# Kernel optimization log

Hardware: AMD Instinct MI355X
Metric: run time of the kernel (lower is better)

The kernel has to match this reference:

```python
import jax, jax.numpy as jnp
import numpy as np

HEADS = 16

def setup_inputs() -> dict:
    key = jax.random.key(0)
    k1, k2, k3 = jax.random.split(key, 3)
    T, B, E = 2048, 4, 1024
    query = jax.random.normal(k1, (T, B, E), dtype=jnp.float32)
    in_proj_weight = jax.random.normal(k2, (3 * E, E), dtype=jnp.float32) * (E ** -0.5)
    out_proj_weight = jax.random.normal(k3, (E, E), dtype=jnp.float32) * (E ** -0.5)
    return {"query": query, "in_proj_weight": in_proj_weight, "out_proj_weight": out_proj_weight}

def reference(query, in_proj_weight, out_proj_weight):
    # query: [T, B, E] (time-first, as in apex SelfMultiheadAttn)
    T, B, E = query.shape
    H = HEADS
    D = E // H
    scale = D ** -0.5
    # fused in-projection: x @ W_in^T -> [T, B, 3E]
    qkv = jnp.einsum('tbe,fe->tbf', query, in_proj_weight)
    q, k, v = jnp.split(qkv, 3, axis=-1)
    # [T, B, E] -> [B, H, T, D]
    def to_bhtd(x):
        return x.reshape(T, B, H, D).transpose(1, 2, 0, 3)
    q = to_bhtd(q) * scale
    k = to_bhtd(k)
    v = to_bhtd(v)
    scores = jnp.einsum('bhqd,bhkd->bhqk', q, k)  # [B, H, T, T]
    # causal (mask_future_timesteps=True) time mask
    causal = jnp.tril(jnp.ones((T, T), dtype=bool))
    scores = jnp.where(causal, scores, jnp.finfo(scores.dtype).min)
    attn = jax.nn.softmax(scores, axis=-1)
    # dropout_prob = 0.0 -> identity
    ctx = jnp.einsum('bhqk,bhkd->bhqd', attn, v)  # [B, H, T, D]
    ctx = ctx.transpose(2, 0, 1, 3).reshape(T, B, E)
    out = jnp.einsum('tbe,fe->tbf', ctx, out_proj_weight)
    return out
```

## Files before the change

### kernel.cpp

```cpp
#include <hip/hip_runtime.h>


typedef float  f32x4  __attribute__((ext_vector_type(4)));
typedef short  s16x8  __attribute__((ext_vector_type(8)));
typedef __bf16 bf16x8 __attribute__((ext_vector_type(8)));

#define T_DIM 2048
#define B_DIM 4
#define E_DIM 1024
#define PLANE (T_DIM * 64)

#define VMC(N) asm volatile("s_waitcnt vmcnt(" #N ")" ::: "memory")
#define LGKM0() asm volatile("s_waitcnt lgkmcnt(0)" ::: "memory")
#define BAR() __builtin_amdgcn_s_barrier()

__device__ inline unsigned short f2bf(float f) {
  return (unsigned short)((__builtin_bit_cast(unsigned int, f) + 0x8000u) >> 16);
}

__device__ inline f32x4 mfma16(s16x8 a, s16x8 b, f32x4 c) {
  return __builtin_amdgcn_mfma_f32_16x16x32_bf16(
      __builtin_bit_cast(bf16x8, a), __builtin_bit_cast(bf16x8, b), c, 0, 0, 0);
}

__device__ inline void gl2lds16(const unsigned short* g, unsigned short* l) {
  __builtin_amdgcn_global_load_lds(
      (__attribute__((address_space(1))) unsigned int*)g,
      (__attribute__((address_space(3))) unsigned int*)l, 16, 0, 0);
}

__device__ inline unsigned packbf(float a, float b) {
  return __builtin_amdgcn_perm(__builtin_bit_cast(unsigned, b),
                               __builtin_bit_cast(unsigned, a), 0x07060302u);
}

__global__ __launch_bounds__(256)
void cvt_all(const float* __restrict__ q, const float* __restrict__ wi,
             const float* __restrict__ wo, unsigned short* __restrict__ xb,
             unsigned short* __restrict__ wib, unsigned short* __restrict__ wob,
             float qs, int do_wout) {
  int blk = blockIdx.x;
  const float* src;
  unsigned short* dst;
  int i;
  float sc = 1.0f;
  if (blk < 8192) {
    src = q; dst = xb; i = blk * 256 + threadIdx.x;
  } else if (blk < 11264) {
    src = wi; dst = wib; i = (blk - 8192) * 256 + threadIdx.x;
    if (i < (E_DIM * E_DIM / 4)) sc = qs;
  } else {
    if (!do_wout) return;
    src = wo; dst = wob; i = (blk - 11264) * 256 + threadIdx.x;
  }
  float4 v = ((const float4*)src)[i];
  ushort4 o;
  o.x = f2bf(v.x * sc); o.y = f2bf(v.y * sc);
  o.z = f2bf(v.z * sc); o.w = f2bf(v.w * sc);
  ((ushort4*)dst)[i] = o;
}

__global__ __launch_bounds__(256)
void cvt_bf16(const float* __restrict__ in, unsigned short* __restrict__ out,
              int n4) {
  int i = blockIdx.x * 256 + threadIdx.x;
  if (i >= n4) return;
  float4 v = ((const float4*)in)[i];
  ushort4 o;
  o.x = f2bf(v.x); o.y = f2bf(v.y); o.z = f2bf(v.z); o.w = f2bf(v.w);
  ((ushort4*)out)[i] = o;
}

__global__ __launch_bounds__(256)
void gemm_qkv(const unsigned short* __restrict__ A,
              const unsigned short* __restrict__ Bw,
              unsigned short* __restrict__ Cq, int K) {
  __shared__ __attribute__((aligned(16))) unsigned short As[2][8192];
  __shared__ __attribute__((aligned(16))) unsigned short Bs[2][8192];

  const int tid = threadIdx.x, lane = tid & 63, w = tid >> 6;
  const int row16 = lane & 15, quad = lane >> 4;
  const int m0 = blockIdx.y * 128, n0 = blockIdx.x * 128;
  const int wm = (w & 1) * 64, wn = (w >> 1) * 64;
  const int srow = lane >> 3;
  const int jsw = (lane & 7) ^ srow;
  const int sw7 = row16 & 7;

  f32x4 acc[4][4];
  for (int i = 0; i < 4; ++i)
    for (int j = 0; j < 4; ++j) acc[i][j] = (f32x4){0.f, 0.f, 0.f, 0.f};

  auto stage = [&](int kt, int buf) {
#pragma unroll
    for (int i = 0; i < 4; ++i) {
      int ia = i * 4 + w;
      int r = ia * 8 + srow;
      gl2lds16(A  + (size_t)(m0 + r) * K + kt * 64 + jsw * 8,
               &As[buf][ia * 512]);
      gl2lds16(Bw + (size_t)(n0 + r) * K + kt * 64 + jsw * 8,
               &Bs[buf][ia * 512]);
    }
  };

  const int NT = K / 64;
  stage(0, 0);
  stage(1, 1);

  for (int kt = 0; kt < NT; ++kt) {
    const int buf = kt & 1;
    if (kt < NT - 1) VMC(8);
    else             VMC(0);
    BAR();

    for (int kk = 0; kk < 2; ++kk) {
      s16x8 af[4], bfr[4];
      for (int mi = 0; mi < 4; ++mi)
        af[mi] = *(const s16x8*)&As[buf][(wm + mi * 16 + row16) * 64 +
                                         (((kk * 4 + quad) ^ sw7) * 8)];
      for (int ni = 0; ni < 4; ++ni)
        bfr[ni] = *(const s16x8*)&Bs[buf][(wn + ni * 16 + row16) * 64 +
                                          (((kk * 4 + quad) ^ sw7) * 8)];
      for (int mi = 0; mi < 4; ++mi)
        for (int ni = 0; ni < 4; ++ni)
          acc[mi][ni] = mfma16(af[mi], bfr[ni], acc[mi][ni]);
    }

    BAR();
    if (kt + 2 < NT) stage(kt + 2, buf);
  }

  if (n0 >= 2048) {
    const int hw = ((n0 - 2048) >> 6) + (w >> 1);
    const int tg0 = (m0 >> 2) + (w & 1) * 16;
    unsigned short* tb = &As[0][0] + w * 1536;
    for (int bb = 0; bb < 4; ++bb) {
#pragma unroll
      for (int mi = 0; mi < 4; ++mi)
#pragma unroll
        for (int ni = 0; ni < 4; ++ni)
          tb[(ni * 16 + row16) * 24 + mi * 4 + quad] = f2bf(acc[mi][ni][bb]);
      LGKM0();
      unsigned short* vp = Cq + (size_t)(128 + bb * 16 + hw) * PLANE;
#pragma unroll
      for (int it = 0; it < 2; ++it) {
        int dd = it * 32 + (lane >> 1);
        int tl = (lane & 1) * 8;
        s16x8 v = *(const s16x8*)&tb[dd * 24 + tl];
        *(s16x8*)(vp + (size_t)dd * T_DIM + tg0 + tl) = v;
      }
      LGKM0();
    }
  } else {
    for (int mi = 0; mi < 4; ++mi)
      for (int ni = 0; ni < 4; ++ni)
        for (int r = 0; r < 4; ++r) {
          int m = m0 + wm + mi * 16 + quad * 4 + r;
          int n = n0 + wn + ni * 16 + row16;
          int t = m >> 2, bb = m & 3;
          int which = n >> 10, hh = (n >> 6) & 15, dd = n & 63;
          Cq[(size_t)(which * 64 + bb * 16 + hh) * PLANE + (size_t)t * 64 + dd] =
              f2bf(acc[mi][ni][r]);
        }
  }
}

__global__ __launch_bounds__(256)
void gemm128(const unsigned short* __restrict__ A,
             const unsigned short* __restrict__ Bw,
             float* __restrict__ Cf, int N, int K) {
  __shared__ __attribute__((aligned(16))) unsigned short As[128 * 64];
  __shared__ __attribute__((aligned(16))) unsigned short Bs[128 * 64];

  const int tid = threadIdx.x, lane = tid & 63, w = tid >> 6;
  const int row16 = lane & 15, quad = lane >> 4;
  const int m0 = blockIdx.y * 128, n0 = blockIdx.x * 128;
  const int wm = (w & 1) * 64, wn = (w >> 1) * 64;
  const int srow = lane >> 3;
  const int jsw = (lane & 7) ^ srow;
  const int sw7 = row16 & 7;

  f32x4 acc[4][4];
  for (int i = 0; i < 4; ++i)
    for (int j = 0; j < 4; ++j) acc[i][j] = (f32x4){0.f, 0.f, 0.f, 0.f};

  for (int k0 = 0; k0 < K; k0 += 64) {
    for (int i = 0; i < 4; ++i) {
      int ia = i * 4 + w;
      int r = ia * 8 + srow;
      gl2lds16(A  + (size_t)(m0 + r) * K + k0 + jsw * 8, &As[ia * 512]);
      gl2lds16(Bw + (size_t)(n0 + r) * K + k0 + jsw * 8, &Bs[ia * 512]);
    }
    __syncthreads();
    for (int kk = 0; kk < 2; ++kk) {
      s16x8 af[4], bfr[4];
      for (int mi = 0; mi < 4; ++mi)
        af[mi] = *(const s16x8*)&As[(wm + mi * 16 + row16) * 64 +
                                    (((kk * 4 + quad) ^ sw7) * 8)];
      for (int ni = 0; ni < 4; ++ni)
        bfr[ni] = *(const s16x8*)&Bs[(wn + ni * 16 + row16) * 64 +
                                     (((kk * 4 + quad) ^ sw7) * 8)];
      for (int mi = 0; mi < 4; ++mi)
        for (int ni = 0; ni < 4; ++ni)
          acc[mi][ni] = mfma16(af[mi], bfr[ni], acc[mi][ni]);
    }
    __syncthreads();
  }

  for (int mi = 0; mi < 4; ++mi)
    for (int ni = 0; ni < 4; ++ni)
      for (int r = 0; r < 4; ++r) {
        int m = m0 + wm + mi * 16 + quad * 4 + r;
        int n = n0 + wn + ni * 16 + row16;
        Cf[(size_t)m * N + n] = acc[mi][ni][r];
      }
}

__global__ __launch_bounds__(512, 4)
void attn_fwd(const unsigned short* __restrict__ qkv,
              unsigned short* __restrict__ ctx) {
  __shared__ __attribute__((aligned(16))) unsigned short Ks[2][4096];
  __shared__ __attribute__((aligned(16))) unsigned short Vs[2][4096];
  __shared__ __attribute__((aligned(16))) unsigned short Ps[8][1024];

  const int tid = threadIdx.x, lane = tid & 63, w = tid >> 6;
  const int row16 = lane & 15, quad = lane >> 4;
  const int bh = blockIdx.x;
  const int p  = blockIdx.y;
  const int b = bh >> 4, h = bh & 15;

  const unsigned short* Qg = qkv + (size_t)bh * PLANE;
  const unsigned short* Kg = qkv + (size_t)(64 + bh) * PLANE;
  const unsigned short* Vt = qkv + (size_t)(128 + bh) * PLANE;

  const int r8 = lane >> 3;
  const int jsw = (lane & 7) ^ r8;
  const int sw7 = row16 & 7;

  auto stage = [&](int c, int buf) {
    int r = w * 8 + r8;
    gl2lds16(Kg + (size_t)(c * 64 + r) * 64 + jsw * 8, &Ks[buf][w * 512]);
    gl2lds16(Vt + (size_t)r * T_DIM + c * 64 + jsw * 8, &Vs[buf][w * 512]);
  };

  for (int half = 0; half < 2; ++half) {
    const int qt = half ? p : (15 - p);
    const int q0w = qt * 128 + w * 16;
    const int cmax = 2 * qt + 1;
    const int dc = 2 * qt + (w >> 2);

    s16x8 qb[2];
    for (int s = 0; s < 2; ++s)
      qb[s] = *(const s16x8*)(Qg + (size_t)(q0w + row16) * 64 + s * 32 +
                              quad * 8);

    f32x4 O[4];
    for (int md = 0; md < 4; ++md) O[md] = (f32x4){0.f, 0.f, 0.f, 0.f};
    float lp = 0.f;

    stage(0, 0);
    stage(1, 1);

    for (int c = 0; c <= cmax; ++c) {
      const int buf = c & 1;
      if (c < cmax) VMC(2);
      else          VMC(0);
      BAR();

      if (c <= dc) {
        f32x4 S[4];
        for (int nt = 0; nt < 4; ++nt) S[nt] = (f32x4){0.f, 0.f, 0.f, 0.f};
        __builtin_amdgcn_s_setprio(1);
        for (int nt = 0; nt < 4; ++nt)
          for (int s = 0; s < 2; ++s) {
            s16x8 ka = *(const s16x8*)&Ks[buf][(nt * 16 + row16) * 64 +
                                              (((s * 4 + quad) ^ sw7) * 8)];
            S[nt] = mfma16(ka, qb[s], S[nt]);
          }
        __builtin_amdgcn_s_setprio(0);

        const int qg = q0w + row16;
        auto softmax_store = [&](bool diagm) {
          for (int nt = 0; nt < 4; ++nt) {
            float pv[4];
            for (int r = 0; r < 4; ++r) {
              pv[r] = __builtin_amdgcn_exp2f(S[nt][r]);
              if (diagm && (c * 64 + nt * 16 + quad * 4 + r) > qg) pv[r] = 0.f;
              lp += pv[r];
            }
            int pos = (nt * 2 + (quad >> 1)) ^ sw7;
            *(uint2*)&Ps[w][row16 * 64 + pos * 8 + (quad & 1) * 4] =
                make_uint2(packbf(pv[0], pv[1]), packbf(pv[2], pv[3]));
          }
        };
        if (c == dc) softmax_store(true); else softmax_store(false);
        LGKM0();

        __builtin_amdgcn_s_setprio(1);
        for (int sk = 0; sk < 2; ++sk) {
          s16x8 pb = *(const s16x8*)&Ps[w][row16 * 64 +
                                          (((sk * 4 + quad) ^ sw7) * 8)];
          for (int md = 0; md < 4; ++md) {
            s16x8 va = *(const s16x8*)&Vs[buf][(md * 16 + row16) * 64 +
                                              (((sk * 4 + quad) ^ sw7) * 8)];
            O[md] = mfma16(va, pb, O[md]);
          }
        }
        __builtin_amdgcn_s_setprio(0);
      }

      BAR();
      if (c + 2 <= cmax) stage(c + 2, buf);
    }

    {
      float s = lp;
      s += __shfl_xor(s, 16);
      s += __shfl_xor(s, 32);
      float inv = 1.f / s;
      const int t = q0w + row16;
      for (int md = 0; md < 4; ++md) {
        unsigned lo = packbf(O[md][0] * inv, O[md][1] * inv);
        unsigned hi = packbf(O[md][2] * inv, O[md][3] * inv);
        *(uint2*)&ctx[((size_t)t * B_DIM + b) * E_DIM + h * 64 + md * 16 +
                      quad * 4] = make_uint2(lo, hi);
      }
    }
  }
}

extern "C" void kernel_launch(void* const* d_in, const int* in_sizes, int n_in,
                              void* d_out, int out_size, void* d_ws,
                              size_t ws_size, hipStream_t stream) {
  const float* query = (const float*)d_in[0];
  const float* win   = (const float*)d_in[1];
  const float* wout  = (const float*)d_in[2];
  float* out = (float*)d_out;

  const size_t qkv_el = (size_t)3 * 64 * PLANE;
  const size_t ctx_el = (size_t)T_DIM * B_DIM * E_DIM;

  unsigned short* qkvb = (unsigned short*)d_ws;
  unsigned short* ctxb = qkvb + qkv_el;
  unsigned short* xb   = ctxb;
  unsigned short* winb = (unsigned short*)d_out;

  const bool big_ws = ws_size >= (qkv_el + ctx_el + (size_t)E_DIM * E_DIM) * 2;
  unsigned short* woutb = big_ws ? (ctxb + ctx_el) : qkvb;

  const float QSCALE = 0.18033688011112042f;

  cvt_all<<<big_ws ? 12288 : 11264, 256, 0, stream>>>(
      query, win, wout, xb, winb, woutb, QSCALE, big_ws ? 1 : 0);
  gemm_qkv<<<dim3(3072 / 128, 8192 / 128), 256, 0, stream>>>(xb, winb, qkvb,
                                                             1024);
  attn_fwd<<<dim3(64, 8), 512, 0, stream>>>(qkvb, ctxb);
  if (!big_ws)
    cvt_bf16<<<1024, 256, 0, stream>>>(wout, woutb, (1024 * 1024) / 4);
  gemm128<<<dim3(8, 64), 256, 0, stream>>>(ctxb, woutb, out, 1024, 1024);
}
```

Measured before the change: 227.3 us.

## Use 8-wave QKV GEMM with MFMA priority and pipeline the out-projection GEMM

The QKV projection GEMM now runs 512 threads per block, each wave owning a 32x64 subtile, with s_setprio raised around the MFMA bursts. The V-transpose epilogue is reworked for the smaller per-wave tile. The output projection GEMM switches from a single-buffered, syncthreads-based loop to the double-buffered async-load pipeline. The aim is higher occupancy and better overlap of loads with MFMA, at the cost of more LDS per block and a lower MFMA-to-LDS-read ratio per wave.

```diff
diff --git a/kernel.cpp b/kernel.cpp
--- a/kernel.cpp
+++ b/kernel.cpp
@@ -71,10 +71,103 @@
   ((ushort4*)out)[i] = o;
 }
 
-__global__ __launch_bounds__(256)
+__global__ __launch_bounds__(512, 4)
 void gemm_qkv(const unsigned short* __restrict__ A,
               const unsigned short* __restrict__ Bw,
               unsigned short* __restrict__ Cq, int K) {
+  __shared__ __attribute__((aligned(16))) unsigned short As[2][8192];
+  __shared__ __attribute__((aligned(16))) unsigned short Bs[2][8192];
+
+  const int tid = threadIdx.x, lane = tid & 63, w = tid >> 6;
+  const int row16 = lane & 15, quad = lane >> 4;
+  const int m0 = blockIdx.y * 128, n0 = blockIdx.x * 128;
+  const int wm = (w & 3) * 32, wn = (w >> 2) * 64;
+  const int srow = lane >> 3;
+  const int jsw = (lane & 7) ^ srow;
+  const int sw7 = row16 & 7;
+
+  f32x4 acc[2][4];
+  for (int i = 0; i < 2; ++i)
+    for (int j = 0; j < 4; ++j) acc[i][j] = (f32x4){0.f, 0.f, 0.f, 0.f};
+
+  auto stage = [&](int kt, int buf) {
+#pragma unroll
+    for (int i = 0; i < 2; ++i) {
+      int ia = w * 2 + i;
+      int r = ia * 8 + srow;
+      gl2lds16(A  + (size_t)(m0 + r) * K + kt * 64 + jsw * 8,
+               &As[buf][ia * 512]);
+      gl2lds16(Bw + (size_t)(n0 + r) * K + kt * 64 + jsw * 8,
+               &Bs[buf][ia * 512]);
+    }
+  };
+
+  const int NT = K / 64;
+  stage(0, 0);
+  stage(1, 1);
+
+  for (int kt = 0; kt < NT; ++kt) {
+    const int buf = kt & 1;
+    if (kt < NT - 1) VMC(4);
+    else             VMC(0);
+    BAR();
+
+    for (int kk = 0; kk < 2; ++kk) {
+      s16x8 af[2], bfr[4];
+      for (int mi = 0; mi < 2; ++mi)
+        af[mi] = *(const s16x8*)&As[buf][(wm + mi * 16 + row16) * 64 +
+                                         (((kk * 4 + quad) ^ sw7) * 8)];
+      for (int ni = 0; ni < 4; ++ni)
+        bfr[ni] = *(const s16x8*)&Bs[buf][(wn + ni * 16 + row16) * 64 +
+                                          (((kk * 4 + quad) ^ sw7) * 8)];
+      __builtin_amdgcn_s_setprio(1);
+      for (int mi = 0; mi < 2; ++mi)
+        for (int ni = 0; ni < 4; ++ni)
+          acc[mi][ni] = mfma16(af[mi], bfr[ni], acc[mi][ni]);
+      __builtin_amdgcn_s_setprio(0);
+    }
+
+    BAR();
+    if (kt + 2 < NT) stage(kt + 2, buf);
+  }
+
+  if (n0 >= 2048) {
+    const int hw = ((n0 - 2048) >> 6) + (w >> 2);
+    const int tg0 = (m0 >> 2) + (w & 3) * 8;
+    unsigned short* tb = &As[0][0] + w * 768;
+    for (int bb = 0; bb < 4; ++bb) {
+#pragma unroll
+      for (int mi = 0; mi < 2; ++mi)
+#pragma unroll
+        for (int ni = 0; ni < 4; ++ni)
+          tb[(ni * 16 + row16) * 12 + mi * 4 + quad] = f2bf(acc[mi][ni][bb]);
+      LGKM0();
+      unsigned short* vp = Cq + (size_t)(128 + bb * 16 + hw) * PLANE;
+      {
+        int dd = lane;
+        s16x8 v = *(const s16x8*)&tb[dd * 12];
+        *(s16x8*)(vp + (size_t)dd * T_DIM + tg0) = v;
+      }
+      LGKM0();
+    }
+  } else {
+    for (int mi = 0; mi < 2; ++mi)
+      for (int ni = 0; ni < 4; ++ni)
+        for (int r = 0; r < 4; ++r) {
+          int m = m0 + wm + mi * 16 + quad * 4 + r;
+          int n = n0 + wn + ni * 16 + row16;
+          int t = m >> 2, bb = m & 3;
+          int which = n >> 10, hh = (n >> 6) & 15, dd = n & 63;
+          Cq[(size_t)(which * 64 + bb * 16 + hh) * PLANE + (size_t)t * 64 + dd] =
+              f2bf(acc[mi][ni][r]);
+        }
+  }
+}
+
+__global__ __launch_bounds__(256)
+void gemm128(const unsigned short* __restrict__ A,
+             const unsigned short* __restrict__ Bw,
+             float* __restrict__ Cf, int N, int K) {
   __shared__ __attribute__((aligned(16))) unsigned short As[2][8192];
   __shared__ __attribute__((aligned(16))) unsigned short Bs[2][8192];
 
@@ -127,83 +220,6 @@
 
     BAR();
     if (kt + 2 < NT) stage(kt + 2, buf);
-  }
-
-  if (n0 >= 2048) {
-    const int hw = ((n0 - 2048) >> 6) + (w >> 1);
-    const int tg0 = (m0 >> 2) + (w & 1) * 16;
-    unsigned short* tb = &As[0][0] + w * 1536;
-    for (int bb = 0; bb < 4; ++bb) {
-#pragma unroll
-      for (int mi = 0; mi < 4; ++mi)
-#pragma unroll
-        for (int ni = 0; ni < 4; ++ni)
-          tb[(ni * 16 + row16) * 24 + mi * 4 + quad] = f2bf(acc[mi][ni][bb]);
-      LGKM0();
-      unsigned short* vp = Cq + (size_t)(128 + bb * 16 + hw) * PLANE;
-#pragma unroll
-      for (int it = 0; it < 2; ++it) {
-        int dd = it * 32 + (lane >> 1);
-        int tl = (lane & 1) * 8;
-        s16x8 v = *(const s16x8*)&tb[dd * 24 + tl];
-        *(s16x8*)(vp + (size_t)dd * T_DIM + tg0 + tl) = v;
-      }
-      LGKM0();
-    }
-  } else {
-    for (int mi = 0; mi < 4; ++mi)
-      for (int ni = 0; ni < 4; ++ni)
-        for (int r = 0; r < 4; ++r) {
-          int m = m0 + wm + mi * 16 + quad * 4 + r;
-          int n = n0 + wn + ni * 16 + row16;
-          int t = m >> 2, bb = m & 3;
-          int which = n >> 10, hh = (n >> 6) & 15, dd = n & 63;
-          Cq[(size_t)(which * 64 + bb * 16 + hh) * PLANE + (size_t)t * 64 + dd] =
-              f2bf(acc[mi][ni][r]);
-        }
-  }
-}
-
-__global__ __launch_bounds__(256)
-void gemm128(const unsigned short* __restrict__ A,
-             const unsigned short* __restrict__ Bw,
-             float* __restrict__ Cf, int N, int K) {
-  __shared__ __attribute__((aligned(16))) unsigned short As[128 * 64];
-  __shared__ __attribute__((aligned(16))) unsigned short Bs[128 * 64];
-
-  const int tid = threadIdx.x, lane = tid & 63, w = tid >> 6;
-  const int row16 = lane & 15, quad = lane >> 4;
-  const int m0 = blockIdx.y * 128, n0 = blockIdx.x * 128;
-  const int wm = (w & 1) * 64, wn = (w >> 1) * 64;
-  const int srow = lane >> 3;
-  const int jsw = (lane & 7) ^ srow;
-  const int sw7 = row16 & 7;
-
-  f32x4 acc[4][4];
-  for (int i = 0; i < 4; ++i)
-    for (int j = 0; j < 4; ++j) acc[i][j] = (f32x4){0.f, 0.f, 0.f, 0.f};
-
-  for (int k0 = 0; k0 < K; k0 += 64) {
-    for (int i = 0; i < 4; ++i) {
-      int ia = i * 4 + w;
-      int r = ia * 8 + srow;
-      gl2lds16(A  + (size_t)(m0 + r) * K + k0 + jsw * 8, &As[ia * 512]);
-      gl2lds16(Bw + (size_t)(n0 + r) * K + k0 + jsw * 8, &Bs[ia * 512]);
-    }
-    __syncthreads();
-    for (int kk = 0; kk < 2; ++kk) {
-      s16x8 af[4], bfr[4];
-      for (int mi = 0; mi < 4; ++mi)
-        af[mi] = *(const s16x8*)&As[(wm + mi * 16 + row16) * 64 +
-                                    (((kk * 4 + quad) ^ sw7) * 8)];
-      for (int ni = 0; ni < 4; ++ni)
-        bfr[ni] = *(const s16x8*)&Bs[(wn + ni * 16 + row16) * 64 +
-                                     (((kk * 4 + quad) ^ sw7) * 8)];
-      for (int mi = 0; mi < 4; ++mi)
-        for (int ni = 0; ni < 4; ++ni)
-          acc[mi][ni] = mfma16(af[mi], bfr[ni], acc[mi][ni]);
-    }
-    __syncthreads();
   }
 
   for (int mi = 0; mi < 4; ++mi)
@@ -351,7 +367,7 @@
 
   cvt_all<<<big_ws ? 12288 : 11264, 256, 0, stream>>>(
       query, win, wout, xb, winb, woutb, QSCALE, big_ws ? 1 : 0);
-  gemm_qkv<<<dim3(3072 / 128, 8192 / 128), 256, 0, stream>>>(xb, winb, qkvb,
+  gemm_qkv<<<dim3(3072 / 128, 8192 / 128), 512, 0, stream>>>(xb, winb, qkvb,
                                                              1024);
   attn_fwd<<<dim3(64, 8), 512, 0, stream>>>(qkvb, ctxb);
   if (!big_ws)
```

New measurement: 227.2 us. About the same (-0.0%).

## Shrink QKV GEMM K-tile to 32 for occupancy; double-buffer out-proj GEMM

Applied to the files above, without the earlier changes.

The QKV projection GEMM now stages 32-wide K tiles, which halves its LDS footprint. It gets a new XOR swizzle, launch bounds requesting 4 blocks per CU, and s_setprio around the MFMA burst. The output-projection GEMM (gemm128) takes over the previous double-buffered 64-wide pipeline with vmcnt waits in place of its single-buffered __syncthreads loop. The aim is more resident waves for the QKV GEMM and overlap of loads with compute in the out-projection. The trade-off is twice as many barriers per K in the QKV GEMM and more LDS in gemm128.

```diff
diff --git a/kernel.cpp b/kernel.cpp
--- a/kernel.cpp
+++ b/kernel.cpp
@@ -71,10 +71,102 @@
   ((ushort4*)out)[i] = o;
 }
 
-__global__ __launch_bounds__(256)
+__global__ __launch_bounds__(256, 4)
 void gemm_qkv(const unsigned short* __restrict__ A,
               const unsigned short* __restrict__ Bw,
               unsigned short* __restrict__ Cq, int K) {
+  __shared__ __attribute__((aligned(16))) unsigned short As[2][4096];
+  __shared__ __attribute__((aligned(16))) unsigned short Bs[2][4096];
+
+  const int tid = threadIdx.x, lane = tid & 63, w = tid >> 6;
+  const int row16 = lane & 15, quad = lane >> 4;
+  const int m0 = blockIdx.y * 128, n0 = blockIdx.x * 128;
+  const int wm = (w & 1) * 64, wn = (w >> 1) * 64;
+  const int jsw = (lane & 3) ^ ((lane >> 3) & 3);
+  const int csw = (row16 >> 1) & 3;
+
+  f32x4 acc[4][4];
+  for (int i = 0; i < 4; ++i)
+    for (int j = 0; j < 4; ++j) acc[i][j] = (f32x4){0.f, 0.f, 0.f, 0.f};
+
+  auto stage = [&](int kt, int buf) {
+#pragma unroll
+    for (int i = 0; i < 2; ++i) {
+      int ia = i * 4 + w;
+      int r = ia * 16 + (lane >> 2);
+      gl2lds16(A  + (size_t)(m0 + r) * K + kt * 32 + jsw * 8,
+               &As[buf][ia * 512]);
+      gl2lds16(Bw + (size_t)(n0 + r) * K + kt * 32 + jsw * 8,
+               &Bs[buf][ia * 512]);
+    }
+  };
+
+  const int NT = K / 32;
+  stage(0, 0);
+  stage(1, 1);
+
+  for (int kt = 0; kt < NT; ++kt) {
+    const int buf = kt & 1;
+    if (kt < NT - 1) VMC(4);
+    else             VMC(0);
+    BAR();
+
+    s16x8 af[4], bfr[4];
+    for (int mi = 0; mi < 4; ++mi)
+      af[mi] = *(const s16x8*)&As[buf][(wm + mi * 16 + row16) * 32 +
+                                       ((quad ^ csw) * 8)];
+    for (int ni = 0; ni < 4; ++ni)
+      bfr[ni] = *(const s16x8*)&Bs[buf][(wn + ni * 16 + row16) * 32 +
+                                        ((quad ^ csw) * 8)];
+    __builtin_amdgcn_s_setprio(1);
+    for (int mi = 0; mi < 4; ++mi)
+      for (int ni = 0; ni < 4; ++ni)
+        acc[mi][ni] = mfma16(af[mi], bfr[ni], acc[mi][ni]);
+    __builtin_amdgcn_s_setprio(0);
+
+    BAR();
+    if (kt + 2 < NT) stage(kt + 2, buf);
+  }
+
+  if (n0 >= 2048) {
+    const int hw = ((n0 - 2048) >> 6) + (w >> 1);
+    const int tg0 = (m0 >> 2) + (w & 1) * 16;
+    unsigned short* tb = &As[0][0] + w * 1536;
+    for (int bb = 0; bb < 4; ++bb) {
+#pragma unroll
+      for (int mi = 0; mi < 4; ++mi)
+#pragma unroll
+        for (int ni = 0; ni < 4; ++ni)
+          tb[(ni * 16 + row16) * 24 + mi * 4 + quad] = f2bf(acc[mi][ni][bb]);
+      LGKM0();
+      unsigned short* vp = Cq + (size_t)(128 + bb * 16 + hw) * PLANE;
+#pragma unroll
+      for (int it = 0; it < 2; ++it) {
+        int dd = it * 32 + (lane >> 1);
+        int tl = (lane & 1) * 8;
+        s16x8 v = *(const s16x8*)&tb[dd * 24 + tl];
+        *(s16x8*)(vp + (size_t)dd * T_DIM + tg0 + tl) = v;
+      }
+      LGKM0();
+    }
+  } else {
+    for (int mi = 0; mi < 4; ++mi)
+      for (int ni = 0; ni < 4; ++ni)
+        for (int r = 0; r < 4; ++r) {
+          int m = m0 + wm + mi * 16 + quad * 4 + r;
+          int n = n0 + wn + ni * 16 + row16;
+          int t = m >> 2, bb = m & 3;
+          int which = n >> 10, hh = (n >> 6) & 15, dd = n & 63;
+          Cq[(size_t)(which * 64 + bb * 16 + hh) * PLANE + (size_t)t * 64 + dd] =
+              f2bf(acc[mi][ni][r]);
+        }
+  }
+}
+
+__global__ __launch_bounds__(256)
+void gemm128(const unsigned short* __restrict__ A,
+             const unsigned short* __restrict__ Bw,
+             float* __restrict__ Cf, int N, int K) {
   __shared__ __attribute__((aligned(16))) unsigned short As[2][8192];
   __shared__ __attribute__((aligned(16))) unsigned short Bs[2][8192];
 
@@ -127,83 +219,6 @@
 
     BAR();
     if (kt + 2 < NT) stage(kt + 2, buf);
-  }
-
-  if (n0 >= 2048) {
-    const int hw = ((n0 - 2048) >> 6) + (w >> 1);
-    const int tg0 = (m0 >> 2) + (w & 1) * 16;
-    unsigned short* tb = &As[0][0] + w * 1536;
-    for (int bb = 0; bb < 4; ++bb) {
-#pragma unroll
-      for (int mi = 0; mi < 4; ++mi)
-#pragma unroll
-        for (int ni = 0; ni < 4; ++ni)
-          tb[(ni * 16 + row16) * 24 + mi * 4 + quad] = f2bf(acc[mi][ni][bb]);
-      LGKM0();
-      unsigned short* vp = Cq + (size_t)(128 + bb * 16 + hw) * PLANE;
-#pragma unroll
-      for (int it = 0; it < 2; ++it) {
-        int dd = it * 32 + (lane >> 1);
-        int tl = (lane & 1) * 8;
-        s16x8 v = *(const s16x8*)&tb[dd * 24 + tl];
-        *(s16x8*)(vp + (size_t)dd * T_DIM + tg0 + tl) = v;
-      }
-      LGKM0();
-    }
-  } else {
-    for (int mi = 0; mi < 4; ++mi)
-      for (int ni = 0; ni < 4; ++ni)
-        for (int r = 0; r < 4; ++r) {
-          int m = m0 + wm + mi * 16 + quad * 4 + r;
-          int n = n0 + wn + ni * 16 + row16;
-          int t = m >> 2, bb = m & 3;
-          int which = n >> 10, hh = (n >> 6) & 15, dd = n & 63;
-          Cq[(size_t)(which * 64 + bb * 16 + hh) * PLANE + (size_t)t * 64 + dd] =
-              f2bf(acc[mi][ni][r]);
-        }
-  }
-}
-
-__global__ __launch_bounds__(256)
-void gemm128(const unsigned short* __restrict__ A,
-             const unsigned short* __restrict__ Bw,
-             float* __restrict__ Cf, int N, int K) {
-  __shared__ __attribute__((aligned(16))) unsigned short As[128 * 64];
-  __shared__ __attribute__((aligned(16))) unsigned short Bs[128 * 64];
-
-  const int tid = threadIdx.x, lane = tid & 63, w = tid >> 6;
-  const int row16 = lane & 15, quad = lane >> 4;
-  const int m0 = blockIdx.y * 128, n0 = blockIdx.x * 128;
-  const int wm = (w & 1) * 64, wn = (w >> 1) * 64;
-  const int srow = lane >> 3;
-  const int jsw = (lane & 7) ^ srow;
-  const int sw7 = row16 & 7;
-
-  f32x4 acc[4][4];
-  for (int i = 0; i < 4; ++i)
-    for (int j = 0; j < 4; ++j) acc[i][j] = (f32x4){0.f, 0.f, 0.f, 0.f};
-
-  for (int k0 = 0; k0 < K; k0 += 64) {
-    for (int i = 0; i < 4; ++i) {
-      int ia = i * 4 + w;
-      int r = ia * 8 + srow;
-      gl2lds16(A  + (size_t)(m0 + r) * K + k0 + jsw * 8, &As[ia * 512]);
-      gl2lds16(Bw + (size_t)(n0 + r) * K + k0 + jsw * 8, &Bs[ia * 512]);
-    }
-    __syncthreads();
-    for (int kk = 0; kk < 2; ++kk) {
-      s16x8 af[4], bfr[4];
-      for (int mi = 0; mi < 4; ++mi)
-        af[mi] = *(const s16x8*)&As[(wm + mi * 16 + row16) * 64 +
-                                    (((kk * 4 + quad) ^ sw7) * 8)];
-      for (int ni = 0; ni < 4; ++ni)
-        bfr[ni] = *(const s16x8*)&Bs[(wn + ni * 16 + row16) * 64 +
-                                     (((kk * 4 + quad) ^ sw7) * 8)];
-      for (int mi = 0; mi < 4; ++mi)
-        for (int ni = 0; ni < 4; ++ni)
-          acc[mi][ni] = mfma16(af[mi], bfr[ni], acc[mi][ni]);
-    }
-    __syncthreads();
   }
 
   for (int mi = 0; mi < 4; ++mi)
```

Result: no change. 230.5 us (+1.4%).
